# Kernel optimization log

Hardware: AMD Instinct MI355X
Metric: run time of the kernel (lower is better)

Reference implementation:

```python
import jax, jax.numpy as jnp
import numpy as np
from jax import lax

B, CIN, CH, HW, K = 256, 256, 256, 16, 3


def setup_inputs() -> dict:
    key = jax.random.key(0)
    ks = jax.random.split(key, 9)
    s = 0.05
    return {
        "x": jax.random.normal(ks[0], (B, CIN, HW, HW), dtype=jnp.float32),
        "h": jax.random.normal(ks[1], (B, CH, HW, HW), dtype=jnp.float32),
        "c": jax.random.normal(ks[2], (B, CH, HW, HW), dtype=jnp.float32),
        # stacked x-branch conv weights for gates [i, f, c, o]; no bias (matches torch code)
        "Wx": jax.random.normal(ks[3], (4 * CH, CIN, K, K), dtype=jnp.float32) * s,
        # stacked h-branch conv weights for gates [i, f, c, o]; with bias
        "Wh": jax.random.normal(ks[4], (4 * CH, CH, K, K), dtype=jnp.float32) * s,
        "bh": jax.random.normal(ks[5], (4 * CH,), dtype=jnp.float32) * s,
        # peephole params (torch inits them to zeros; use small randn to exercise the math)
        "Wci": jax.random.normal(ks[6], (1, CH, HW, HW), dtype=jnp.float32) * s,
        "Wcf": jax.random.normal(ks[7], (1, CH, HW, HW), dtype=jnp.float32) * s,
        "Wco": jax.random.normal(ks[8], (1, CH, HW, HW), dtype=jnp.float32) * s,
    }


def _conv(x, w):
    # same-padding 2D conv, NCHW/OIHW
    return lax.conv_general_dilated(
        x, w, window_strides=(1, 1), padding="SAME",
        dimension_numbers=("NCHW", "OIHW", "NCHW"))


def reference(x, h, c, Wx, Wh, bh, Wci, Wcf, Wco):
    gx = _conv(x, Wx)                                   # [B, 4*CH, H, W]
    gh = _conv(h, Wh) + bh[None, :, None, None]         # [B, 4*CH, H, W]
    xi, xf, xc, xo = jnp.split(gx, 4, axis=1)
    hi, hf, hc, ho = jnp.split(gh, 4, axis=1)
    i_t = jax.nn.sigmoid(xi + hi + Wci * c)
    f_t = jax.nn.sigmoid(xf + hf + Wcf * c)
    c_t = f_t * c + i_t * jnp.tanh(xc + hc)
    o_t = jax.nn.sigmoid(xo + ho + Wco * c_t)
    h_t = o_t * jnp.tanh(c_t)
    return (h_t, c_t)
```

## Files before the change

kernel.cpp:

```cpp
#include <hip/hip_runtime.h>


typedef __bf16 bf16x8 __attribute__((ext_vector_type(8)));
typedef float f32x16 __attribute__((ext_vector_type(16)));

#define PLANE_B  20736u
#define XH_BYTES (4096u * PLANE_B)
#define OUT_HALF 16777216u

__device__ inline void gload_lds16(const void* g, void* l) {
    __builtin_amdgcn_global_load_lds(
        (const __attribute__((address_space(1))) void*)g,
        (__attribute__((address_space(3))) void*)l, 16, 0, 0);
}

__global__ __launch_bounds__(256) void xh_transform(
    const float* __restrict__ x, const float* __restrict__ hh,
    unsigned char* __restrict__ xh)
{
    int blk = blockIdx.x;
    int b = blk >> 4, ibk = blk & 15;
    const float* src = (ibk < 8) ? (x  + ((size_t)(b*256 + ibk*32)) * 256)
                                 : (hh + ((size_t)(b*256 + (ibk-8)*32)) * 256);
    int t = threadIdx.x;
    uint32_t w[16];
#pragma unroll
    for (int i = 0; i < 16; ++i) {
        __bf16 lo = (__bf16)src[(size_t)(2*i  )*256 + t];
        __bf16 hi = (__bf16)src[(size_t)(2*i+1)*256 + t];
        w[i] = (uint32_t)__builtin_bit_cast(unsigned short, lo)
             | ((uint32_t)__builtin_bit_cast(unsigned short, hi) << 16);
    }
    unsigned char* plane = xh + (size_t)blk * PLANE_B;
    int p = ((t >> 4) + 1)*18 + (t & 15) + 1;
    uint32_t key  = (uint32_t)(p & 7) << 4;
    uint32_t base = (uint32_t)p * 64u;
#pragma unroll
    for (int k = 0; k < 4; ++k)
        *(uint4*)(plane + ((base + 16u*k) ^ key)) =
            uint4{w[4*k], w[4*k+1], w[4*k+2], w[4*k+3]};
    if (t < 68) {
        int pb;
        if      (t < 18) pb = t;
        else if (t < 36) pb = 17*18 + (t - 18);
        else if (t < 52) pb = (t - 35)*18;
        else             pb = (t - 51)*18 + 17;
        uint32_t kb = (uint32_t)(pb & 7) << 4;
        uint32_t bb = (uint32_t)pb * 64u;
        uint4 z{0u,0u,0u,0u};
#pragma unroll
        for (int k = 0; k < 4; ++k)
            *(uint4*)(plane + ((bb + 16u*k) ^ kb)) = z;
    }
}

__global__ __launch_bounds__(256) void w_transform(
    const float* __restrict__ Wx, const float* __restrict__ Wh,
    __bf16* __restrict__ Wt)
{
    int idx  = blockIdx.x * 256 + threadIdx.x;
    int lane = idx & 63;
    int chunk = idx >> 6;
    int half  = chunk & 1;
    int icblk = (chunk >> 1) & 15;
    int fg    = (chunk >> 5) & 3;
    int cb    = (chunk >> 7) & 7;
    int pos   = chunk >> 10;
    int row = lane & 31, hl = lane >> 5;
    int gate = row & 3, ch8 = row >> 2;
    int oc  = gate*256 + cb*32 + fg*8 + ch8;
    int ic0 = icblk*32 + half*16 + hl*8;
    bf16x8 v;
#pragma unroll
    for (int j = 0; j < 8; ++j) {
        int ic = ic0 + j;
        float w = (ic < 256) ? Wx[((size_t)oc*256 + ic      )*9 + pos]
                             : Wh[((size_t)oc*256 + (ic-256))*9 + pos];
        v[j] = (__bf16)w;
    }
    *(bf16x8*)(Wt + (size_t)chunk*512 + (size_t)lane*8) = v;
}

__global__ __launch_bounds__(256, 2) void convlstm_main(
    const unsigned char* __restrict__ xh, const __bf16* __restrict__ Wt,
    const float* __restrict__ bh,  const float* __restrict__ cin,
    const float* __restrict__ Wci, const float* __restrict__ Wcf,
    const float* __restrict__ Wco, float* __restrict__ out)
{
    int bid = blockIdx.x;
    int cb  = bid & 7;
    int nh  = (bid >> 3) & 1;
    int b   = bid >> 4;
    int tid = threadIdx.x;
    int lane = tid & 63, wv = tid >> 6;
    int l31 = lane & 31, hl = lane >> 5;

    __shared__ __align__(16) unsigned char lds[2][24576];

    f32x16 acc[2][2];
#pragma unroll
    for (int f = 0; f < 2; ++f) {
        int fg = nh*2 + f;
        f32x16 v;
#pragma unroll
        for (int r = 0; r < 16; ++r) {
            int gate = r & 3, q = r >> 2;
            v[r] = bh[gate*256 + cb*32 + fg*8 + 2*q + hl];
        }
        acc[0][f] = v; acc[1][f] = v;
    }

    const unsigned char* planes = xh + (size_t)b * (16u * PLANE_B);

#pragma unroll
    for (int k = 0; k < 6; ++k)
        gload_lds16(planes + (size_t)(wv*6 + k)*1024u + (size_t)lane*16u,
                    &lds[0][(wv*6 + k)*1024 + lane*16]);

    int m0 = wv*64 + l31,       m1 = wv*64 + 32 + l31;
    int pbase0 = (m0 >> 4)*18 + (m0 & 15);
    int pbase1 = (m1 >> 4)*18 + (m1 & 15);
    const uint32_t kbase = (uint32_t)(hl*16);

    const __bf16* wlane = Wt + (size_t)lane * 8;
    auto achunk = [&](int ibk, int ph, int f) -> size_t {
        int pos = ph >> 1, half = ph & 1, fg = nh*2 + f;
        return ((size_t)((pos*8 + cb)*4 + fg))*32 + (size_t)(ibk*2 + half);
    };
    auto bread = [&](const unsigned char* rb, int pbase, int ph) -> bf16x8 {
        int pos = ph >> 1, half = ph & 1;
        int p = pbase + (pos/3)*18 + (pos%3);
        uint32_t byte = ((uint32_t)p*64u + kbase + (uint32_t)(half*32))
                        ^ (((uint32_t)(p & 7)) << 4);
        return *(const bf16x8*)(rb + byte);
    };

    bf16x8 A[3][2];
#pragma unroll
    for (int f = 0; f < 2; ++f) {
        A[0][f] = *(const bf16x8*)(wlane + achunk(0, 0, f)*512);
        A[1][f] = *(const bf16x8*)(wlane + achunk(0, 1, f)*512);
    }

    __syncthreads();

    for (int ibk = 0; ibk < 16; ++ibk) {
        const unsigned char* rb = lds[ibk & 1];

        bf16x8 Bb[2][2];
        Bb[0][0] = bread(rb, pbase0, 0);
        Bb[0][1] = bread(rb, pbase1, 0);

#pragma unroll
        for (int p = 0; p < 18; ++p) {
            {
                int tp  = p + 2;
                int nib = (tp < 18) ? ibk : ((ibk < 15) ? ibk + 1 : 15);
                int nph = (tp < 18) ? tp : tp - 18;
#pragma unroll
                for (int f = 0; f < 2; ++f)
                    A[(p+2)%3][f] =
                        *(const bf16x8*)(wlane + achunk(nib, nph, f)*512);
            }
            if (p == 1 && ibk < 15) {
                const unsigned char* np = planes + (size_t)(ibk+1) * PLANE_B;
#pragma unroll
                for (int k = 0; k < 6; ++k)
                    gload_lds16(np + (size_t)(wv*6 + k)*1024u
                                   + (size_t)lane*16u,
                                &lds[(ibk & 1) ^ 1][(wv*6 + k)*1024 + lane*16]);
            }
            if (p < 17) {
                Bb[(p+1)&1][0] = bread(rb, pbase0, p+1);
                Bb[(p+1)&1][1] = bread(rb, pbase1, p+1);
            }
            __builtin_amdgcn_s_setprio(1);
            acc[0][0] = __builtin_amdgcn_mfma_f32_32x32x16_bf16(A[p%3][0], Bb[p&1][0], acc[0][0], 0, 0, 0);
            acc[0][1] = __builtin_amdgcn_mfma_f32_32x32x16_bf16(A[p%3][1], Bb[p&1][0], acc[0][1], 0, 0, 0);
            acc[1][0] = __builtin_amdgcn_mfma_f32_32x32x16_bf16(A[p%3][0], Bb[p&1][1], acc[1][0], 0, 0, 0);
            acc[1][1] = __builtin_amdgcn_mfma_f32_32x32x16_bf16(A[p%3][1], Bb[p&1][1], acc[1][1], 0, 0, 0);
            __builtin_amdgcn_s_setprio(0);
        }

        asm volatile("s_waitcnt vmcnt(4) lgkmcnt(0)" ::: "memory");
        __builtin_amdgcn_s_barrier();
        __builtin_amdgcn_sched_barrier(0);
    }

    float* outh = out;
    float* outc = out + (size_t)OUT_HALF;
    const size_t bOff = (size_t)b * (256*256);
#pragma unroll
    for (int mf = 0; mf < 2; ++mf) {
        int m = wv*64 + mf*32 + l31;
#pragma unroll
        for (int f = 0; f < 2; ++f) {
            int fg = nh*2 + f;
#pragma unroll
            for (int q = 0; q < 4; ++q) {
                int ch = cb*32 + fg*8 + 2*q + hl;
                size_t pidx = (size_t)ch*256 + (size_t)m;
                size_t idx  = bOff + pidx;
                float cv = cin[idx];
                float pi = acc[mf][f][4*q+0];
                float pf = acc[mf][f][4*q+1];
                float pc = acc[mf][f][4*q+2];
                float po = acc[mf][f][4*q+3];
                float it = 1.f/(1.f + __expf(-(pi + Wci[pidx]*cv)));
                float ft = 1.f/(1.f + __expf(-(pf + Wcf[pidx]*cv)));
                float tc = 1.f - 2.f/(1.f + __expf(2.f*pc));
                float ct = ft*cv + it*tc;
                float ot = 1.f/(1.f + __expf(-(po + Wco[pidx]*ct)));
                float th = 1.f - 2.f/(1.f + __expf(2.f*ct));
                outh[idx] = ot*th;
                outc[idx] = ct;
            }
        }
    }
}

extern "C" void kernel_launch(void* const* d_in, const int* in_sizes, int n_in,
                              void* d_out, int out_size, void* d_ws, size_t ws_size,
                              hipStream_t stream)
{
    const float* x   = (const float*)d_in[0];
    const float* h   = (const float*)d_in[1];
    const float* c   = (const float*)d_in[2];
    const float* Wx  = (const float*)d_in[3];
    const float* Wh  = (const float*)d_in[4];
    const float* bh  = (const float*)d_in[5];
    const float* Wci = (const float*)d_in[6];
    const float* Wcf = (const float*)d_in[7];
    const float* Wco = (const float*)d_in[8];
    float* out = (float*)d_out;

    unsigned char* xh = (unsigned char*)d_ws;
    __bf16* Wt = (__bf16*)(xh + (size_t)XH_BYTES + 4096);

    hipLaunchKernelGGL(xh_transform, dim3(4096), dim3(256), 0, stream, x, h, xh);
    hipLaunchKernelGGL(w_transform,  dim3(2304), dim3(256), 0, stream, Wx, Wh, Wt);
    hipLaunchKernelGGL(convlstm_main, dim3(4096), dim3(256), 0, stream,
                       xh, Wt, bh, c, Wci, Wcf, Wco, out);
}
```

Measured before the change: 626.4 us.

## Reorder weight layout for contiguous per-block streaming and precompute LDS addresses

Changes the transformed weight layout so each (cb, nh) block's A-operand stream is contiguous in consumption order, letting the main loop use a single base pointer with constant offsets. Precomputes swizzled LDS B-read addresses per tap once and flips between double buffers by adding a constant. Peels the last input-channel block to remove per-iteration conditionals. This is meant to cut scalar/vector address arithmetic in the MFMA inner loop, at the cost of more live registers for the address table.

After: 630.9 us. Within noise of the previous version (+0.7%).

```diff
diff --git a/kernel.cpp b/kernel.cpp
--- a/kernel.cpp
+++ b/kernel.cpp
@@ -61,15 +61,17 @@
     int idx  = blockIdx.x * 256 + threadIdx.x;
     int lane = idx & 63;
     int chunk = idx >> 6;
-    int half  = chunk & 1;
-    int icblk = (chunk >> 1) & 15;
-    int fg    = (chunk >> 5) & 3;
-    int cb    = (chunk >> 7) & 7;
-    int pos   = chunk >> 10;
+    int f     = chunk & 1;
+    int half  = (chunk >> 1) & 1;
+    int pos   = (chunk >> 2) % 9;
+    int rest  = (chunk >> 2) / 9;
+    int ibk   = rest & 15;
+    int cbnh  = rest >> 4;
+    int nh = cbnh & 1, cb = cbnh >> 1;
     int row = lane & 31, hl = lane >> 5;
     int gate = row & 3, ch8 = row >> 2;
-    int oc  = gate*256 + cb*32 + fg*8 + ch8;
-    int ic0 = icblk*32 + half*16 + hl*8;
+    int oc  = gate*256 + cb*32 + (nh*2 + f)*8 + ch8;
+    int ic0 = ibk*32 + half*16 + hl*8;
     bf16x8 v;
 #pragma unroll
     for (int j = 0; j < 8; ++j) {
@@ -117,75 +119,92 @@
         gload_lds16(planes + (size_t)(wv*6 + k)*1024u + (size_t)lane*16u,
                     &lds[0][(wv*6 + k)*1024 + lane*16]);
 
-    int m0 = wv*64 + l31,       m1 = wv*64 + 32 + l31;
-    int pbase0 = (m0 >> 4)*18 + (m0 & 15);
-    int pbase1 = (m1 >> 4)*18 + (m1 & 15);
+    int m0 = wv*64 + l31, m1 = m0 + 32;
+    int pb0 = (m0 >> 4)*18 + (m0 & 15);
+    int pb1 = (m1 >> 4)*18 + (m1 & 15);
     const uint32_t kbase = (uint32_t)(hl*16);
-
-    const __bf16* wlane = Wt + (size_t)lane * 8;
-    auto achunk = [&](int ibk, int ph, int f) -> size_t {
-        int pos = ph >> 1, half = ph & 1, fg = nh*2 + f;
-        return ((size_t)((pos*8 + cb)*4 + fg))*32 + (size_t)(ibk*2 + half);
-    };
-    auto bread = [&](const unsigned char* rb, int pbase, int ph) -> bf16x8 {
-        int pos = ph >> 1, half = ph & 1;
-        int p = pbase + (pos/3)*18 + (pos%3);
-        uint32_t byte = ((uint32_t)p*64u + kbase + (uint32_t)(half*32))
-                        ^ (((uint32_t)(p & 7)) << 4);
-        return *(const bf16x8*)(rb + byte);
-    };
+    uint32_t baddr[9][2];
+#pragma unroll
+    for (int pos = 0; pos < 9; ++pos) {
+        int d = (pos/3)*18 + (pos%3);
+        int p0 = pb0 + d, p1 = pb1 + d;
+        baddr[pos][0] = ((uint32_t)p0*64u + kbase) ^ (((uint32_t)(p0 & 7)) << 4);
+        baddr[pos][1] = ((uint32_t)p1*64u + kbase) ^ (((uint32_t)(p1 & 7)) << 4);
+    }
+    const char* lds0 = (const char*)&lds[0][0];
+
+    const __bf16* abase = Wt + (size_t)(cb*2 + nh)*294912u + (size_t)lane*8;
 
     bf16x8 A[3][2];
-#pragma unroll
-    for (int f = 0; f < 2; ++f) {
-        A[0][f] = *(const bf16x8*)(wlane + achunk(0, 0, f)*512);
-        A[1][f] = *(const bf16x8*)(wlane + achunk(0, 1, f)*512);
-    }
+    A[0][0] = *(const bf16x8*)(abase + 0);
+    A[0][1] = *(const bf16x8*)(abase + 512);
+    A[1][0] = *(const bf16x8*)(abase + 1024);
+    A[1][1] = *(const bf16x8*)(abase + 1536);
 
     __syncthreads();
 
-    for (int ibk = 0; ibk < 16; ++ibk) {
-        const unsigned char* rb = lds[ibk & 1];
-
-        bf16x8 Bb[2][2];
-        Bb[0][0] = bread(rb, pbase0, 0);
-        Bb[0][1] = bread(rb, pbase1, 0);
-
-#pragma unroll
-        for (int p = 0; p < 18; ++p) {
-            {
-                int tp  = p + 2;
-                int nib = (tp < 18) ? ibk : ((ibk < 15) ? ibk + 1 : 15);
-                int nph = (tp < 18) ? tp : tp - 18;
-#pragma unroll
-                for (int f = 0; f < 2; ++f)
-                    A[(p+2)%3][f] =
-                        *(const bf16x8*)(wlane + achunk(nib, nph, f)*512);
-            }
-            if (p == 1 && ibk < 15) {
-                const unsigned char* np = planes + (size_t)(ibk+1) * PLANE_B;
-#pragma unroll
-                for (int k = 0; k < 6; ++k)
-                    gload_lds16(np + (size_t)(wv*6 + k)*1024u
-                                   + (size_t)lane*16u,
-                                &lds[(ibk & 1) ^ 1][(wv*6 + k)*1024 + lane*16]);
-            }
-            if (p < 17) {
-                Bb[(p+1)&1][0] = bread(rb, pbase0, p+1);
-                Bb[(p+1)&1][1] = bread(rb, pbase1, p+1);
-            }
-            __builtin_amdgcn_s_setprio(1);
-            acc[0][0] = __builtin_amdgcn_mfma_f32_32x32x16_bf16(A[p%3][0], Bb[p&1][0], acc[0][0], 0, 0, 0);
-            acc[0][1] = __builtin_amdgcn_mfma_f32_32x32x16_bf16(A[p%3][1], Bb[p&1][0], acc[0][1], 0, 0, 0);
-            acc[1][0] = __builtin_amdgcn_mfma_f32_32x32x16_bf16(A[p%3][0], Bb[p&1][1], acc[1][0], 0, 0, 0);
-            acc[1][1] = __builtin_amdgcn_mfma_f32_32x32x16_bf16(A[p%3][1], Bb[p&1][1], acc[1][1], 0, 0, 0);
-            __builtin_amdgcn_s_setprio(0);
+#define IBK_PHASES(LAST)                                                     \
+    {                                                                        \
+        bf16x8 Bb[2][2];                                                     \
+        Bb[0][0] = *(const bf16x8*)(lds0 + baddr[0][0]);                     \
+        Bb[0][1] = *(const bf16x8*)(lds0 + baddr[0][1]);                     \
+        _Pragma("unroll")                                                    \
+        for (int p = 0; p < 18; ++p) {                                       \
+              \
+            {                                                                \
+                const int tp = p + 2;                                        \
+                const int xo = (tp < 18) ? 0 : ((LAST) ? -18432 : 0);        \
+                const int off = ((tp < 18)                                   \
+                    ? ((tp>>1)*2048 + (tp&1)*1024)                           \
+                    : (18432 + (((tp-18)>>1)*2048 + ((tp-18)&1)*1024))) + xo;\
+                A[(p+2)%3][0] = *(const bf16x8*)(abase + off);               \
+                A[(p+2)%3][1] = *(const bf16x8*)(abase + off + 512);         \
+            }                                                                \
+            if (p == 1 && !(LAST)) {                                         \
+                const unsigned char* np_ = planes + (size_t)(ibk+1)*PLANE_B; \
+                _Pragma("unroll")                                            \
+                for (int k = 0; k < 6; ++k)                                  \
+                    gload_lds16(np_ + (size_t)(wv*6 + k)*1024u               \
+                                    + (size_t)lane*16u,                      \
+                                &lds[(ibk & 1) ^ 1][(wv*6 + k)*1024          \
+                                                    + lane*16]);             \
+            }                                                                \
+            if (p < 17) {                                                    \
+                const int np = p + 1;                                        \
+                uint32_t a0 = baddr[np>>1][0] ^ (uint32_t)((np&1)*32);       \
+                uint32_t a1 = baddr[np>>1][1] ^ (uint32_t)((np&1)*32);       \
+                Bb[np&1][0] = *(const bf16x8*)(lds0 + a0);                   \
+                Bb[np&1][1] = *(const bf16x8*)(lds0 + a1);                   \
+            }                                                                \
+            __builtin_amdgcn_s_setprio(1);                                   \
+            acc[0][0] = __builtin_amdgcn_mfma_f32_32x32x16_bf16(A[p%3][0], Bb[p&1][0], acc[0][0], 0, 0, 0); \
+            acc[0][1] = __builtin_amdgcn_mfma_f32_32x32x16_bf16(A[p%3][1], Bb[p&1][0], acc[0][1], 0, 0, 0); \
+            acc[1][0] = __builtin_amdgcn_mfma_f32_32x32x16_bf16(A[p%3][0], Bb[p&1][1], acc[1][0], 0, 0, 0); \
+            acc[1][1] = __builtin_amdgcn_mfma_f32_32x32x16_bf16(A[p%3][1], Bb[p&1][1], acc[1][1], 0, 0, 0); \
+            __builtin_amdgcn_s_setprio(0);                                   \
+        }                                                                    \
+    }
+
+    int flipd = 24576;
+    for (int ibk = 0; ibk < 15; ++ibk) {
+        IBK_PHASES(0)
+#pragma unroll
+        for (int pos = 0; pos < 9; ++pos) {
+            baddr[pos][0] += (uint32_t)flipd;
+            baddr[pos][1] += (uint32_t)flipd;
         }
-
+        flipd = -flipd;
+        abase += 18432;
         asm volatile("s_waitcnt vmcnt(4) lgkmcnt(0)" ::: "memory");
         __builtin_amdgcn_s_barrier();
         __builtin_amdgcn_sched_barrier(0);
     }
+    {
+        const int ibk = 15;
+        (void)ibk;
+        IBK_PHASES(1)
+    }
+#undef IBK_PHASES
 
     float* outh = out;
     float* outc = out + (size_t)OUT_HALF;
```
